# Kernel optimization log

Measured on AMD Instinct MI355X. Metric: run time of the kernel, lower is better.

The kernel has to match this reference:

```python
import jax, jax.numpy as jnp
import numpy as np

N_SKU, N_WH, N_SUP = 100000, 5000, 2000
D_IN, D_OUT, H = 128, 64, 4
DH = D_OUT // H  # 16
E_INTRA, E_CROSS = 400000, 200000
EPS_LN = 1e-5


def setup_inputs() -> dict:
    key = jax.random.key(0)
    ks = jax.random.split(key, 40)
    f32 = jnp.float32

    def edges(k, E, n_src, n_dst):
        k1, k2 = jax.random.split(k)
        return jnp.stack([
            jax.random.randint(k1, (E,), 0, n_src),
            jax.random.randint(k2, (E,), 0, n_dst),
        ]).astype(jnp.int32)

    inp = {
        'x_sku': jax.random.normal(ks[0], (N_SKU, D_IN), f32),
        'x_wh': jax.random.normal(ks[1], (N_WH, D_IN), f32),
        'x_sup': jax.random.normal(ks[2], (N_SUP, D_IN), f32),
    }
    names = ['plant', 'pg', 'sg', 'st', 'ship', 'supply']
    for i, nm in enumerate(names):
        inp['W_' + nm] = jax.random.normal(ks[3 + 2 * i], (D_IN, D_OUT), f32) * 0.05
        inp['a_' + nm] = jax.random.normal(ks[4 + 2 * i], (2 * DH,), f32) * 0.05
    inp['proj_W'] = jax.random.normal(ks[20], (2 * D_OUT, D_OUT), f32) * 0.05
    inp['proj_b'] = jnp.zeros((D_OUT,), f32)
    inp['ln_g'] = jnp.ones((D_OUT,), f32)
    inp['ln_b'] = jnp.zeros((D_OUT,), f32)
    inp['res_W'] = jax.random.normal(ks[21], (D_IN, D_OUT), f32) * 0.05
    inp['ei_plant'] = edges(ks[22], E_INTRA, N_SKU, N_SKU)
    inp['ei_pg'] = edges(ks[23], E_INTRA, N_SKU, N_SKU)
    inp['ei_sg'] = edges(ks[24], E_INTRA, N_SKU, N_SKU)
    inp['ei_st'] = edges(ks[25], E_INTRA, N_SKU, N_SKU)
    inp['ei_ship'] = edges(ks[26], E_CROSS, N_SKU, N_WH)
    inp['ei_supply'] = edges(ks[27], E_CROSS, N_SKU, N_SUP)
    return inp


def _gat_conv(src_feat, dst_feat, ei, W, a, num_dst):
    """One-edge-type multi-head GAT: ELU edge scores, per-dst softmax, scatter-add."""
    src_i, dst_i = ei[0], ei[1]
    h_src = (src_feat @ W).reshape(-1, H, DH)  # [N_src, H, dh]
    h_dst = (dst_feat @ W).reshape(-1, H, DH)  # [N_dst, H, dh]
    hs = h_src[src_i]  # [E, H, dh] gather
    hd = h_dst[dst_i]  # [E, H, dh]
    # a^T [h_src || h_dst], shared attention vector across heads
    e = jax.nn.elu(hs @ a[:DH] + hd @ a[DH:])  # [E, H]
    # numerically stable scatter-softmax over edges grouped by dst node
    e_max = jax.lax.stop_gradient(jax.ops.segment_max(e, dst_i, num_segments=num_dst))
    e_max = jnp.where(jnp.isfinite(e_max), e_max, 0.0)
    exp_e = jnp.exp(e - e_max[dst_i])
    denom = jax.ops.segment_sum(exp_e, dst_i, num_segments=num_dst)
    alpha = exp_e / (denom[dst_i] + 1e-12)  # [E, H]
    out = jax.ops.segment_sum(alpha[..., None] * hs, dst_i, num_segments=num_dst)
    return out.reshape(num_dst, D_OUT)


def reference(x_sku, x_wh, x_sup,
              W_plant, a_plant, W_pg, a_pg, W_sg, a_sg, W_st, a_st,
              W_ship, a_ship, W_supply, a_supply,
              proj_W, proj_b, ln_g, ln_b, res_W,
              ei_plant, ei_pg, ei_sg, ei_st, ei_ship, ei_supply):
    # branch A (intra sku->sku edge types), summed into sku accumulator
    oa_sku = (_gat_conv(x_sku, x_sku, ei_plant, W_plant, a_plant, N_SKU)
              + _gat_conv(x_sku, x_sku, ei_pg, W_pg, a_pg, N_SKU)
              + _gat_conv(x_sku, x_sku, ei_sg, W_sg, a_sg, N_SKU)
              + _gat_conv(x_sku, x_sku, ei_st, W_st, a_st, N_SKU))
    ob_sku = jnp.zeros((N_SKU, D_OUT), x_sku.dtype)
    # branch B (cross edge types)
    oa_wh = jnp.zeros((N_WH, D_OUT), x_wh.dtype)
    ob_wh = _gat_conv(x_sku, x_wh, ei_ship, W_ship, a_ship, N_WH)
    oa_sup = jnp.zeros((N_SUP, D_OUT), x_sup.dtype)
    ob_sup = _gat_conv(x_sku, x_sup, ei_supply, W_supply, a_supply, N_SUP)

    def finish(x, oa, ob):
        y = jnp.concatenate([oa, ob], axis=-1) @ proj_W + proj_b + x @ res_W
        mu = y.mean(-1, keepdims=True)
        var = ((y - mu) ** 2).mean(-1, keepdims=True)
        return (y - mu) / jnp.sqrt(var + EPS_LN) * ln_g + ln_b

    return (finish(x_sku, oa_sku, ob_sku),
            finish(x_wh, oa_wh, ob_wh),
            finish(x_sup, oa_sup, ob_sup))
```

## Files before the change

### kernel.cpp

```cpp
#include <hip/hip_runtime.h>
#include <hip/hip_bf16.h>
#include <cstdint>

#define NS 100000
#define NW 5000
#define NPS 2000
#define DI 128
#define DO 64
#define NSTRIPS (NS/16)
#define NFLAT (4*NS + NW + NPS)
#define NWPAD 5008
#define NBUK 134
#define BCAP 20480
#define CHUNK 8192

typedef unsigned short bfu;
typedef __attribute__((ext_vector_type(8))) short s8v;
typedef __attribute__((ext_vector_type(4))) float f4v;

__device__ inline bfu f2bf(float f) {
  uint32_t u = __float_as_uint(f);
  u = (u + 0x7FFFu + ((u >> 16) & 1u)) >> 16;
  return (bfu)u;
}
__device__ inline float bf2f(bfu u) {
  return __uint_as_float((uint32_t)u << 16);
}

__global__ void k_convert3(const float* __restrict__ x0, bfu* __restrict__ o0, int n0,
                           const float* __restrict__ x1, bfu* __restrict__ o1, int n1,
                           const float* __restrict__ x2, bfu* __restrict__ o2, int n2) {
  int t = blockIdx.x * 256 + threadIdx.x;
  const float* x; bfu* o; int i;
  if (t < n0) { x = x0; o = o0; i = t; }
  else if (t < n0 + n1) { x = x1; o = o1; i = t - n0; }
  else if (t < n0 + n1 + n2) { x = x2; o = o2; i = t - n0 - n1; }
  else return;
  const float4* p = (const float4*)x + (size_t)i * 2;
  float4 a = p[0], b = p[1];
  uint4 v;
  v.x = (uint32_t)f2bf(a.x) | ((uint32_t)f2bf(a.y) << 16);
  v.y = (uint32_t)f2bf(a.z) | ((uint32_t)f2bf(a.w) << 16);
  v.z = (uint32_t)f2bf(b.x) | ((uint32_t)f2bf(b.y) << 16);
  v.w = (uint32_t)f2bf(b.z) | ((uint32_t)f2bf(b.w) << 16);
  ((uint4*)o)[i] = v;
}

struct PackArgs {
  const float* W[6]; const float* a[6];
  const float* resW; const float* projW;
  bfu* Bp; bfu* Rp; bfu* Pp;
  float* wv_wh; float* wv_sup;
};
__global__ void k_pack_all(PackArgs P) {
  int t = blockIdx.x * 256 + threadIdx.x;
  if (t < 61440) {
    int ty = t / 10240, rem = t % 10240;
    int r = rem / 128, k = rem % 128;
    const float* W = P.W[ty]; const float* a = P.a[ty];
    float v = 0.f;
    if (r < 64) v = W[k * 64 + r];
    else if (r < 72) {
      int h = (r - 64) & 3;
      const float* av = (r < 68) ? a : (a + 16);
      #pragma unroll
      for (int m = 0; m < 16; ++m) v += W[k * 64 + h * 16 + m] * av[m];
    }
    P.Bp[ty * 10240 + rem] = f2bf(v);
  } else if (t < 69632) {
    int i = t - 61440; int j = i / 128, k = i % 128;
    P.Rp[i] = f2bf(P.resW[k * 64 + j]);
  } else if (t < 77824) {
    int i = t - 69632; int j = i / 128, k = i % 128;
    P.Pp[i] = f2bf(P.projW[k * 64 + j]);
  } else if (t < 78848) {
    int i = t - 77824; int which = i / 512;
    int k = (i % 512) / 4, h = i % 4;
    const float* W = P.W[4 + which]; const float* a = P.a[4 + which];
    float v = 0.f;
    #pragma unroll
    for (int m = 0; m < 16; ++m) v += W[k * 64 + h * 16 + m] * a[16 + m];
    (which ? P.wv_sup : P.wv_wh)[k * 4 + h] = v;
  }
}

__global__ __launch_bounds__(256, 2) void k_gemm2t(const bfu* __restrict__ xb,
    const bfu* __restrict__ Bp0, const bfu* __restrict__ Bp1,
    bfu* __restrict__ hb0, bfu* __restrict__ hb1,
    float* __restrict__ ss0, float* __restrict__ ss1,
    float* __restrict__ sd0, float* __restrict__ sd1, int nstrips) {
  int lane = threadIdx.x & 63;
  int l15 = lane & 15, q = lane >> 4;
  int w  = (int)((blockIdx.x * blockDim.x + threadIdx.x) >> 6);
  int nw = (int)((gridDim.x * blockDim.x) >> 6);
  s8v bfr[10][4];
  #pragma unroll
  for (int nt = 0; nt < 5; ++nt)
    #pragma unroll
    for (int kq = 0; kq < 4; ++kq) {
      bfr[nt][kq]     = *(const s8v*)(Bp0 + (size_t)(nt * 16 + l15) * 128 + kq * 32 + q * 8);
      bfr[5 + nt][kq] = *(const s8v*)(Bp1 + (size_t)(nt * 16 + l15) * 128 + kq * 32 + q * 8);
    }
  for (int s = w; s < nstrips; s += nw) {
    int mb = s * 16;
    f4v acc[10];
    #pragma unroll
    for (int u = 0; u < 10; ++u) acc[u] = (f4v){0.f, 0.f, 0.f, 0.f};
    const bfu* ar = xb + (size_t)(mb + l15) * 128 + q * 8;
    #pragma unroll
    for (int kq = 0; kq < 4; ++kq) {
      s8v af = *(const s8v*)(ar + kq * 32);
      #pragma unroll
      for (int u = 0; u < 10; ++u)
        acc[u] = __builtin_amdgcn_mfma_f32_16x16x32_bf16(af, bfr[u][kq], acc[u], 0, 0, 0);
    }
    #pragma unroll
    for (int u = 0; u < 10; ++u) {
      int nt = (u < 5) ? u : u - 5;
      bfu* hb = (u < 5) ? hb0 : hb1;
      float* ssrc = (u < 5) ? ss0 : ss1;
      float* sdst = (u < 5) ? sd0 : sd1;
      int c = nt * 16 + l15;
      #pragma unroll
      for (int r = 0; r < 4; ++r) {
        int node = mb + q * 4 + r;
        float v = acc[u][r];
        if (c < 64)      hb[(size_t)node * 64 + c] = f2bf(v);
        else if (c < 68) ssrc[(size_t)node * 4 + (c - 64)] = v;
        else if (c < 72) sdst[(size_t)node * 4 + (c - 68)] = v;
      }
    }
  }
}

__global__ __launch_bounds__(256) void k_scores(const float* __restrict__ x,
    const float* __restrict__ wv, float* __restrict__ sdst, int N) {
  int lane = threadIdx.x & 63;
  int w  = (int)((blockIdx.x * 256 + threadIdx.x) >> 6);
  int nw = (int)((gridDim.x * 256) >> 6);
  float4 wa = ((const float4*)wv)[lane];
  float4 wb = ((const float4*)wv)[64 + lane];
  for (int n = w; n < N; n += nw) {
    float xa = x[(size_t)n * 128 + lane], xc = x[(size_t)n * 128 + 64 + lane];
    float4 a;
    a.x = xa * wa.x + xc * wb.x; a.y = xa * wa.y + xc * wb.y;
    a.z = xa * wa.z + xc * wb.z; a.w = xa * wa.w + xc * wb.w;
    #pragma unroll
    for (int m = 1; m < 64; m <<= 1) {
      a.x += __shfl_xor(a.x, m); a.y += __shfl_xor(a.y, m);
      a.z += __shfl_xor(a.z, m); a.w += __shfl_xor(a.w, m);
    }
    if (lane == 0) ((float4*)sdst)[n] = a;
  }
}

struct ESeg { const int* ei[6]; int E[6]; int Ecum[7]; };

__device__ inline void buk_of(int t, int d, int& b, int& loc) {
  if (t < 4)       { int f = d * 4 + t; b = f >> 12;        loc = f & 4095; }
  else if (t == 4) { b = 98 + (d >> 8);                     loc = d & 255; }
  else             { b = 118 + (d >> 7);                    loc = d & 127; }
}

__global__ void k_init_cur(int* __restrict__ gCur) {
  int t = threadIdx.x;
  if (t < NBUK) gCur[t] = t * BCAP;
}

__global__ __launch_bounds__(256) void k_bin(ESeg S, int* __restrict__ gCur,
                                             uint32_t* __restrict__ binned, int ETOT) {
  __shared__ int cnt[NBUK];
  __shared__ int runb[NBUK];
  int tid = threadIdx.x;
  int gbase = blockIdx.x * CHUNK;
  if (tid < NBUK) cnt[tid] = 0;
  __syncthreads();
  #pragma unroll 4
  for (int i = 0; i < CHUNK / 256; ++i) {
    int g = gbase + i * 256 + tid;
    if (g < ETOT) {
      int t = 0;
      #pragma unroll
      for (int k = 0; k < 5; ++k) t += (g >= S.Ecum[k + 1]);
      int e = g - S.Ecum[t];
      int d = S.ei[t][S.E[t] + e];
      int b, loc; buk_of(t, d, b, loc);
      atomicAdd(&cnt[b], 1);
    }
  }
  __syncthreads();
  if (tid < NBUK) { runb[tid] = atomicAdd(&gCur[tid], cnt[tid]); cnt[tid] = 0; }
  __syncthreads();
  #pragma unroll 4
  for (int i = 0; i < CHUNK / 256; ++i) {
    int g = gbase + i * 256 + tid;
    if (g < ETOT) {
      int t = 0;
      #pragma unroll
      for (int k = 0; k < 5; ++k) t += (g >= S.Ecum[k + 1]);
      int e = g - S.Ecum[t];
      int sv = S.ei[t][e];
      int d  = S.ei[t][S.E[t] + e];
      int b, loc; buk_of(t, d, b, loc);
      int pos = runb[b] + atomicAdd(&cnt[b], 1);
      if (pos < (b + 1) * BCAP)
        binned[pos] = ((uint32_t)loc << 17) | (uint32_t)sv;
    }
  }
}

__global__ __launch_bounds__(1024) void k_csr(const int* __restrict__ gCur,
    const uint32_t* __restrict__ binned, int* __restrict__ offs,
    int* __restrict__ ssorted) {
  __shared__ int hist[4096];
  __shared__ int wsc[16];
  __shared__ int bbase_s, cnt_s;
  int b = blockIdx.x, tid = threadIdx.x;
  int lane = tid & 63, wid = tid >> 6;
  if (tid == 0) {
    int bb = 0, own = 0;
    for (int k = 0; k < NBUK; ++k) {
      int c = min(gCur[k] - k * BCAP, BCAP);
      if (k < b) bb += c;
      if (k == b) own = c;
    }
    bbase_s = bb; cnt_s = own;
  }
  #pragma unroll
  for (int k = 0; k < 4; ++k) hist[tid * 4 + k] = 0;
  __syncthreads();
  int cnt = cnt_s, bbase = bbase_s;
  const uint32_t* bk = binned + (size_t)b * BCAP;
  for (int i = tid; i < cnt; i += 1024)
    atomicAdd(&hist[bk[i] >> 17], 1);
  __syncthreads();
  int t4 = tid * 4;
  int v0 = hist[t4], v1 = hist[t4 + 1], v2 = hist[t4 + 2], v3 = hist[t4 + 3];
  int tsum = v0 + v1 + v2 + v3;
  int inc = tsum;
  #pragma unroll
  for (int d = 1; d < 64; d <<= 1) { int tt = __shfl_up(inc, d); if (lane >= d) inc += tt; }
  if (lane == 63) wsc[wid] = inc;
  __syncthreads();
  int wpre = 0;
  for (int k = 0; k < wid; ++k) wpre += wsc[k];
  int excl = inc - tsum + wpre;
  hist[t4] = excl;
  hist[t4 + 1] = excl + v0;
  hist[t4 + 2] = excl + v0 + v1;
  hist[t4 + 3] = excl + v0 + v1 + v2;
  __syncthreads();
  int sbase, nslots;
  if (b < 98)        { sbase = b << 12;                nslots = min(4096, 4 * NS - sbase); }
  else if (b < 118)  { int lb = (b - 98) << 8;  sbase = 4 * NS + lb;      nslots = min(256, NW - lb); }
  else               { int lb = (b - 118) << 7; sbase = 4 * NS + NW + lb; nslots = min(128, NPS - lb); }
  for (int i = tid; i < nslots; i += 1024) offs[sbase + i] = bbase + hist[i];
  if (b == NBUK - 1 && tid == 0) offs[NFLAT] = bbase + cnt;
  __syncthreads();
  for (int i = tid; i < cnt; i += 1024) {
    uint32_t v = bk[i];
    int p = atomicAdd(&hist[v >> 17], 1);
    ssorted[bbase + p] = (int)(v & 0x1FFFFu);
  }
}

struct AggArgs {
  const int* offs; const int* srcs;
  const bfu* hbAll;
  const float* ssAll;
  const float* sdAll;
  const float* sd_wh; const float* sd_sup;
  bfu* osku; bfu* owh; bfu* osup;
};

__global__ __launch_bounds__(256) void k_megaagg(AggArgs A) {
  int lane = threadIdx.x & 63, h = lane >> 4;
  int w  = (int)((blockIdx.x * 256 + threadIdx.x) >> 6);
  int nw = (int)((gridDim.x * 256) >> 6);
  for (int n = w; n < NS + NW + NPS; n += nw) {
    float r; bfu* op;
    if (n < NS) {
      const int* ob = A.offs + (size_t)n * 4;
      int4 o = *(const int4*)ob;
      int o4 = ob[4];
      int beg = o.x;
      int b1 = o.y - beg, b2 = o.z - beg, b3 = o.w - beg;
      int tot = o4 - beg;
      float sdv0 = A.sdAll[(size_t)(0 * NS + n) * 4 + h];
      float sdv1 = A.sdAll[(size_t)(1 * NS + n) * 4 + h];
      float sdv2 = A.sdAll[(size_t)(2 * NS + n) * 4 + h];
      float sdv3 = A.sdAll[(size_t)(3 * NS + n) * 4 + h];
      float acc0 = 0.f, acc1 = 0.f, acc2 = 0.f, acc3 = 0.f;
      float den0 = 0.f, den1 = 0.f, den2 = 0.f, den3 = 0.f;
      for (int cb = 0; cb < tot; cb += 64) {
        int rem = min(64, tot - cb);
        int sidx = (lane < rem) ? A.srcs[beg + cb + lane] : 0;
        int j = 0;
        for (; j + 8 <= rem; j += 8) {
          float sc[8]; bfu hv[8]; int tv[8];
          #pragma unroll
          for (int i = 0; i < 8; ++i) {
            int p = cb + j + i;
            int t = (p >= b1) + (p >= b2) + (p >= b3);
            int s = __shfl(sidx, j + i);
            size_t nb = (size_t)t * NS + s;
            sc[i] = A.ssAll[nb * 4 + h];
            hv[i] = A.hbAll[nb * 64 + lane];
            tv[i] = t;
          }
          #pragma unroll
          for (int i = 0; i < 8; ++i) {
            float sdv = (tv[i] == 0) ? sdv0 : (tv[i] == 1) ? sdv1 : (tv[i] == 2) ? sdv2 : sdv3;
            float e = sc[i] + sdv;
            e = e > 0.f ? e : (__expf(e) - 1.f);
            float wgt = __expf(e);
            float hw = bf2f(hv[i]) * wgt;
            if (tv[i] == 0)      { den0 += wgt; acc0 += hw; }
            else if (tv[i] == 1) { den1 += wgt; acc1 += hw; }
            else if (tv[i] == 2) { den2 += wgt; acc2 += hw; }
            else                 { den3 += wgt; acc3 += hw; }
          }
        }
        for (; j < rem; ++j) {
          int p = cb + j;
          int t = (p >= b1) + (p >= b2) + (p >= b3);
          int s = __shfl(sidx, j);
          size_t nb = (size_t)t * NS + s;
          float sc = A.ssAll[nb * 4 + h];
          float hvf = bf2f(A.hbAll[nb * 64 + lane]);
          float sdv = (t == 0) ? sdv0 : (t == 1) ? sdv1 : (t == 2) ? sdv2 : sdv3;
          float e = sc + sdv;
          e = e > 0.f ? e : (__expf(e) - 1.f);
          float wgt = __expf(e);
          float hw = hvf * wgt;
          if (t == 0)      { den0 += wgt; acc0 += hw; }
          else if (t == 1) { den1 += wgt; acc1 += hw; }
          else if (t == 2) { den2 += wgt; acc2 += hw; }
          else             { den3 += wgt; acc3 += hw; }
        }
      }
      r = acc0 / (den0 + 1e-12f) + acc1 / (den1 + 1e-12f)
        + acc2 / (den2 + 1e-12f) + acc3 / (den3 + 1e-12f);
      op = A.osku + (size_t)n * 64;
    } else {
      int tt, nl, fi; const float* sd;
      if (n < NS + NW) { tt = 4; nl = n - NS; fi = 4 * NS + nl; sd = A.sd_wh; op = A.owh + (size_t)nl * 64; }
      else { tt = 5; nl = n - NS - NW; fi = 4 * NS + NW + nl; sd = A.sd_sup; op = A.osup + (size_t)nl * 64; }
      int beg = A.offs[fi], end = A.offs[fi + 1];
      const bfu* hb = A.hbAll + (size_t)tt * NS * 64;
      const float* ss = A.ssAll + (size_t)tt * NS * 4;
      float sdv = sd[(size_t)nl * 4 + h];
      float acc = 0.f, den = 0.f;
      for (int cb = beg; cb < end; cb += 64) {
        int rem = min(64, end - cb);
        int sidx = (lane < rem) ? A.srcs[cb + lane] : 0;
        int j = 0;
        for (; j + 8 <= rem; j += 8) {
          float sc[8]; bfu hv[8];
          #pragma unroll
          for (int i = 0; i < 8; ++i) {
            int s = __shfl(sidx, j + i);
            sc[i] = ss[(size_t)s * 4 + h];
            hv[i] = hb[(size_t)s * 64 + lane];
          }
          #pragma unroll
          for (int i = 0; i < 8; ++i) {
            float e = sc[i] + sdv;
            e = e > 0.f ? e : (__expf(e) - 1.f);
            float wgt = __expf(e);
            den += wgt; acc += bf2f(hv[i]) * wgt;
          }
        }
        for (; j < rem; ++j) {
          int s = __shfl(sidx, j);
          float e = ss[(size_t)s * 4 + h] + sdv;
          float hvf = bf2f(hb[(size_t)s * 64 + lane]);
          e = e > 0.f ? e : (__expf(e) - 1.f);
          float wgt = __expf(e);
          den += wgt; acc += hvf * wgt;
        }
      }
      r = acc / (den + 1e-12f);
    }
    op[lane] = f2bf(r);
  }
}

__global__ __launch_bounds__(256) void k_finishM(const bfu* __restrict__ aggb,
    const bfu* __restrict__ xbf, const bfu* __restrict__ Pp, int koff,
    const bfu* __restrict__ Rp, const float* __restrict__ pb,
    const float* __restrict__ g, const float* __restrict__ bb,
    float* __restrict__ outp, int N, int nstrips) {
  int lane = threadIdx.x & 63, l15 = lane & 15, q = lane >> 4;
  int w  = (int)((blockIdx.x * 256 + threadIdx.x) >> 6);
  int nw = (int)((gridDim.x * 256) >> 6);
  s8v bP[4][2], bR[4][4];
  float pbv[4], gv[4], bv[4];
  #pragma unroll
  for (int c = 0; c < 4; ++c) {
    const bfu* pr = Pp + (size_t)(c * 16 + l15) * 128 + koff;
    bP[c][0] = *(const s8v*)(pr + q * 8);
    bP[c][1] = *(const s8v*)(pr + 32 + q * 8);
    const bfu* rr = Rp + (size_t)(c * 16 + l15) * 128;
    #pragma unroll
    for (int kq = 0; kq < 4; ++kq) bR[c][kq] = *(const s8v*)(rr + kq * 32 + q * 8);
    pbv[c] = pb[c * 16 + l15]; gv[c] = g[c * 16 + l15]; bv[c] = bb[c * 16 + l15];
  }
  for (int s = w; s < nstrips; s += nw) {
    int mb = s * 16;
    const bfu* ar = aggb + (size_t)(mb + l15) * 64 + q * 8;
    const bfu* xr = xbf + (size_t)(mb + l15) * 128 + q * 8;
    s8v a0 = *(const s8v*)ar, a1 = *(const s8v*)(ar + 32);
    s8v x0 = *(const s8v*)xr, x1 = *(const s8v*)(xr + 32),
        x2 = *(const s8v*)(xr + 64), x3 = *(const s8v*)(xr + 96);
    f4v acc[4];
    #pragma unroll
    for (int c = 0; c < 4; ++c) {
      acc[c] = (f4v){0.f, 0.f, 0.f, 0.f};
      acc[c] = __builtin_amdgcn_mfma_f32_16x16x32_bf16(a0, bP[c][0], acc[c], 0, 0, 0);
      acc[c] = __builtin_amdgcn_mfma_f32_16x16x32_bf16(a1, bP[c][1], acc[c], 0, 0, 0);
      acc[c] = __builtin_amdgcn_mfma_f32_16x16x32_bf16(x0, bR[c][0], acc[c], 0, 0, 0);
      acc[c] = __builtin_amdgcn_mfma_f32_16x16x32_bf16(x1, bR[c][1], acc[c], 0, 0, 0);
      acc[c] = __builtin_amdgcn_mfma_f32_16x16x32_bf16(x2, bR[c][2], acc[c], 0, 0, 0);
      acc[c] = __builtin_amdgcn_mfma_f32_16x16x32_bf16(x3, bR[c][3], acc[c], 0, 0, 0);
    }
    #pragma unroll
    for (int r = 0; r < 4; ++r) {
      int row = mb + q * 4 + r;
      float y0 = acc[0][r] + pbv[0], y1 = acc[1][r] + pbv[1];
      float y2 = acc[2][r] + pbv[2], y3 = acc[3][r] + pbv[3];
      float s1 = y0 + y1 + y2 + y3;
      s1 += __shfl_xor(s1, 1); s1 += __shfl_xor(s1, 2);
      s1 += __shfl_xor(s1, 4); s1 += __shfl_xor(s1, 8);
      float mu = s1 * 0.015625f;
      float d0 = y0 - mu, d1 = y1 - mu, d2 = y2 - mu, d3 = y3 - mu;
      float s2 = d0 * d0 + d1 * d1 + d2 * d2 + d3 * d3;
      s2 += __shfl_xor(s2, 1); s2 += __shfl_xor(s2, 2);
      s2 += __shfl_xor(s2, 4); s2 += __shfl_xor(s2, 8);
      float rs = rsqrtf(s2 * 0.015625f + 1e-5f);
      if (row < N) {
        float* orow = outp + (size_t)row * 64 + l15;
        orow[0]  = d0 * rs * gv[0] + bv[0];
        orow[16] = d1 * rs * gv[1] + bv[1];
        orow[32] = d2 * rs * gv[2] + bv[2];
        orow[48] = d3 * rs * gv[3] + bv[3];
      }
    }
  }
}

extern "C" void kernel_launch(void* const* d_in, const int* in_sizes, int n_in,
                              void* d_out, int out_size, void* d_ws, size_t ws_size,
                              hipStream_t stream) {
  const float* x_sku = (const float*)d_in[0];
  const float* x_wh  = (const float*)d_in[1];
  const float* x_sup = (const float*)d_in[2];
  const float* Wt[6]; const float* at[6];
  for (int t = 0; t < 6; ++t) { Wt[t] = (const float*)d_in[3 + 2 * t]; at[t] = (const float*)d_in[4 + 2 * t]; }
  const float* projW = (const float*)d_in[15];
  const float* projb = (const float*)d_in[16];
  const float* lng   = (const float*)d_in[17];
  const float* lnb   = (const float*)d_in[18];
  const float* resW  = (const float*)d_in[19];
  const int* ei[6]; int Et[6];
  for (int t = 0; t < 6; ++t) { ei[t] = (const int*)d_in[20 + t]; Et[t] = in_sizes[20 + t] / 2; }
  float* out = (float*)d_out;

  int ETOT = 0;
  for (int t = 0; t < 6; ++t) ETOT += Et[t];

  char* ws = (char*)d_ws;
  size_t off = 0;
  auto alloc = [&](size_t bytes) { off = (off + 255) & ~(size_t)255; void* p = ws + off; off += bytes; return p; };

  bfu*  xb      = (bfu*)alloc((size_t)NS * DI * 2);
  bfu*  xb_wh   = (bfu*)alloc((size_t)NWPAD * DI * 2);
  bfu*  xb_sup  = (bfu*)alloc((size_t)NPS * DI * 2);
  bfu*  Bp      = (bfu*)alloc((size_t)6 * 80 * 128 * 2);
  bfu*  Rp      = (bfu*)alloc((size_t)64 * 128 * 2);
  bfu*  Pp      = (bfu*)alloc((size_t)64 * 128 * 2);
  float* wv_wh  = (float*)alloc(128 * 4 * 4);
  float* wv_sup = (float*)alloc(128 * 4 * 4);
  bfu*  hbAll   = (bfu*)alloc((size_t)6 * NS * 64 * 2);
  float* ssAll  = (float*)alloc((size_t)6 * NS * 4 * 4);
  float* sdAll  = (float*)alloc((size_t)6 * NS * 4 * 4);
  float* sdst_wh  = (float*)alloc((size_t)NW * 4 * 4);
  float* sdst_sup = (float*)alloc((size_t)NPS * 4 * 4);
  size_t agg_bytes = ((size_t)NS + NWPAD + NPS) * 64 * 2;
  size_t bin_bytes = (size_t)NBUK * BCAP * 4;
  char* un = (char*)alloc(agg_bytes > bin_bytes ? agg_bytes : bin_bytes);
  bfu* agg_sku = (bfu*)un;
  bfu* agg_wh  = agg_sku + (size_t)NS * 64;
  bfu* agg_sup = agg_wh + (size_t)NWPAD * 64;
  uint32_t* binned = (uint32_t*)un;
  int* gCur    = (int*)alloc(256 * 4);
  int* offsb   = (int*)alloc((size_t)(NFLAT + 1) * 4);
  int* ssorted = (int*)alloc((size_t)ETOT * 4);

  int n0 = NS * 16, n1 = NW * 16, n2 = NPS * 16;
  k_convert3<<<(n0 + n1 + n2 + 255) / 256, 256, 0, stream>>>(x_sku, xb, n0, x_wh, xb_wh, n1,
                                                             x_sup, xb_sup, n2);

  PackArgs PA;
  for (int t = 0; t < 6; ++t) { PA.W[t] = Wt[t]; PA.a[t] = at[t]; }
  PA.resW = resW; PA.projW = projW; PA.Bp = Bp; PA.Rp = Rp; PA.Pp = Pp;
  PA.wv_wh = wv_wh; PA.wv_sup = wv_sup;
  k_pack_all<<<(78848 + 255) / 256, 256, 0, stream>>>(PA);

  k_scores<<<1250, 256, 0, stream>>>(x_wh, wv_wh, sdst_wh, NW);
  k_scores<<<500, 256, 0, stream>>>(x_sup, wv_sup, sdst_sup, NPS);

  ESeg S;
  S.Ecum[0] = 0;
  for (int t = 0; t < 6; ++t) { S.ei[t] = ei[t]; S.E[t] = Et[t]; S.Ecum[t + 1] = S.Ecum[t] + Et[t]; }
  k_init_cur<<<1, 256, 0, stream>>>(gCur);
  k_bin<<<(ETOT + CHUNK - 1) / CHUNK, 256, 0, stream>>>(S, gCur, binned, ETOT);
  k_csr<<<NBUK, 1024, 0, stream>>>(gCur, binned, offsb, ssorted);

  for (int p = 0; p < 3; ++p) {
    int t0 = 2 * p, t1 = 2 * p + 1;
    k_gemm2t<<<512, 256, 0, stream>>>(xb, Bp + (size_t)t0 * 10240, Bp + (size_t)t1 * 10240,
        hbAll + (size_t)t0 * NS * 64, hbAll + (size_t)t1 * NS * 64,
        ssAll + (size_t)t0 * NS * 4, ssAll + (size_t)t1 * NS * 4,
        sdAll + (size_t)t0 * NS * 4, sdAll + (size_t)t1 * NS * 4, NSTRIPS);
  }

  AggArgs A;
  A.offs = offsb; A.srcs = ssorted;
  A.hbAll = hbAll; A.ssAll = ssAll; A.sdAll = sdAll;
  A.sd_wh = sdst_wh; A.sd_sup = sdst_sup;
  A.osku = agg_sku; A.owh = agg_wh; A.osup = agg_sup;
  k_megaagg<<<(NS + NW + NPS + 3) / 4, 256, 0, stream>>>(A);

  k_finishM<<<1563, 256, 0, stream>>>(agg_sku, xb, Pp, 0, Rp, projb, lng, lnb, out, NS, NSTRIPS);
  k_finishM<<<79, 256, 0, stream>>>(agg_wh, xb_wh, Pp, 64, Rp, projb, lng, lnb,
                                    out + (size_t)NS * 64, NW, NWPAD / 16);
  k_finishM<<<32, 256, 0, stream>>>(agg_sup, xb_sup, Pp, 64, Rp, projb, lng, lnb,
                                    out + (size_t)(NS + NW) * 64, NPS, NPS / 16);
}
```

Before: 464.6 us.

## Split wavefront into quarter-waves processing edge types in parallel with vector loads

The aggregation kernel now maps each 16-lane quarter of a wavefront to one edge type (for SKU nodes) or to interleaved edges (for cross nodes). Each lane loads four bf16 features at once via uint2 and accumulates four channels, and partial sums are combined with cross-quarter shuffles. This replaces the per-edge type selection and serial walk over all edges with four concurrent streams of wider gathers. The cost is padding up to the longest edge-type list, predicated work on short lists, and an extra shuffle reduction at the end.

```diff
diff --git a/kernel.cpp b/kernel.cpp
--- a/kernel.cpp
+++ b/kernel.cpp
@@ -274,115 +274,112 @@
 };
 
 __global__ __launch_bounds__(256) void k_megaagg(AggArgs A) {
-  int lane = threadIdx.x & 63, h = lane >> 4;
+  int lane = threadIdx.x & 63;
+  int q = lane >> 4, m = lane & 15, h = m >> 2;
+  int qsh = q << 4;
   int w  = (int)((blockIdx.x * 256 + threadIdx.x) >> 6);
   int nw = (int)((gridDim.x * 256) >> 6);
   for (int n = w; n < NS + NW + NPS; n += nw) {
-    float r; bfu* op;
     if (n < NS) {
       const int* ob = A.offs + (size_t)n * 4;
       int4 o = *(const int4*)ob;
       int o4 = ob[4];
-      int beg = o.x;
-      int b1 = o.y - beg, b2 = o.z - beg, b3 = o.w - beg;
-      int tot = o4 - beg;
-      float sdv0 = A.sdAll[(size_t)(0 * NS + n) * 4 + h];
-      float sdv1 = A.sdAll[(size_t)(1 * NS + n) * 4 + h];
-      float sdv2 = A.sdAll[(size_t)(2 * NS + n) * 4 + h];
-      float sdv3 = A.sdAll[(size_t)(3 * NS + n) * 4 + h];
-      float acc0 = 0.f, acc1 = 0.f, acc2 = 0.f, acc3 = 0.f;
-      float den0 = 0.f, den1 = 0.f, den2 = 0.f, den3 = 0.f;
-      for (int cb = 0; cb < tot; cb += 64) {
-        int rem = min(64, tot - cb);
-        int sidx = (lane < rem) ? A.srcs[beg + cb + lane] : 0;
-        int j = 0;
-        for (; j + 8 <= rem; j += 8) {
-          float sc[8]; bfu hv[8]; int tv[8];
+      int sb = (q == 0) ? o.x : (q == 1) ? o.y : (q == 2) ? o.z : o.w;
+      int se = (q == 0) ? o.y : (q == 1) ? o.z : (q == 2) ? o.w : o4;
+      int len = se - sb;
+      int maxlen = max(max(o.y - o.x, o.z - o.y), max(o.w - o.z, o4 - o.w));
+      float sdv = A.sdAll[((size_t)q * NS + n) * 4 + h];
+      uint32_t tbase = (uint32_t)q * (uint32_t)NS;
+      float den = 0.f, a0 = 0.f, a1 = 0.f, a2 = 0.f, a3 = 0.f;
+      for (int j0 = 0; j0 < maxlen; j0 += 16) {
+        int ei = j0 + m;
+        int sidx = (ei < len) ? A.srcs[sb + ei] : 0;
+        int gmax = min(16, maxlen - j0);
+        for (int jj = 0; jj < gmax; jj += 8) {
+          float sc[8]; uint2 hv[8]; int vj[8];
           #pragma unroll
           for (int i = 0; i < 8; ++i) {
-            int p = cb + j + i;
-            int t = (p >= b1) + (p >= b2) + (p >= b3);
-            int s = __shfl(sidx, j + i);
-            size_t nb = (size_t)t * NS + s;
-            sc[i] = A.ssAll[nb * 4 + h];
-            hv[i] = A.hbAll[nb * 64 + lane];
-            tv[i] = t;
-          }
-          #pragma unroll
-          for (int i = 0; i < 8; ++i) {
-            float sdv = (tv[i] == 0) ? sdv0 : (tv[i] == 1) ? sdv1 : (tv[i] == 2) ? sdv2 : sdv3;
-            float e = sc[i] + sdv;
-            e = e > 0.f ? e : (__expf(e) - 1.f);
-            float wgt = __expf(e);
-            float hw = bf2f(hv[i]) * wgt;
-            if (tv[i] == 0)      { den0 += wgt; acc0 += hw; }
-            else if (tv[i] == 1) { den1 += wgt; acc1 += hw; }
-            else if (tv[i] == 2) { den2 += wgt; acc2 += hw; }
-            else                 { den3 += wgt; acc3 += hw; }
-          }
-        }
-        for (; j < rem; ++j) {
-          int p = cb + j;
-          int t = (p >= b1) + (p >= b2) + (p >= b3);
-          int s = __shfl(sidx, j);
-          size_t nb = (size_t)t * NS + s;
-          float sc = A.ssAll[nb * 4 + h];
-          float hvf = bf2f(A.hbAll[nb * 64 + lane]);
-          float sdv = (t == 0) ? sdv0 : (t == 1) ? sdv1 : (t == 2) ? sdv2 : sdv3;
-          float e = sc + sdv;
-          e = e > 0.f ? e : (__expf(e) - 1.f);
-          float wgt = __expf(e);
-          float hw = hvf * wgt;
-          if (t == 0)      { den0 += wgt; acc0 += hw; }
-          else if (t == 1) { den1 += wgt; acc1 += hw; }
-          else if (t == 2) { den2 += wgt; acc2 += hw; }
-          else             { den3 += wgt; acc3 += hw; }
-        }
-      }
-      r = acc0 / (den0 + 1e-12f) + acc1 / (den1 + 1e-12f)
-        + acc2 / (den2 + 1e-12f) + acc3 / (den3 + 1e-12f);
-      op = A.osku + (size_t)n * 64;
-    } else {
-      int tt, nl, fi; const float* sd;
-      if (n < NS + NW) { tt = 4; nl = n - NS; fi = 4 * NS + nl; sd = A.sd_wh; op = A.owh + (size_t)nl * 64; }
-      else { tt = 5; nl = n - NS - NW; fi = 4 * NS + NW + nl; sd = A.sd_sup; op = A.osup + (size_t)nl * 64; }
-      int beg = A.offs[fi], end = A.offs[fi + 1];
-      const bfu* hb = A.hbAll + (size_t)tt * NS * 64;
-      const float* ss = A.ssAll + (size_t)tt * NS * 4;
-      float sdv = sd[(size_t)nl * 4 + h];
-      float acc = 0.f, den = 0.f;
-      for (int cb = beg; cb < end; cb += 64) {
-        int rem = min(64, end - cb);
-        int sidx = (lane < rem) ? A.srcs[cb + lane] : 0;
-        int j = 0;
-        for (; j + 8 <= rem; j += 8) {
-          float sc[8]; bfu hv[8];
-          #pragma unroll
-          for (int i = 0; i < 8; ++i) {
-            int s = __shfl(sidx, j + i);
-            sc[i] = ss[(size_t)s * 4 + h];
-            hv[i] = hb[(size_t)s * 64 + lane];
+            int j = jj + i;
+            int s = __shfl(sidx, qsh + j);
+            vj[i] = (j0 + j) < len;
+            uint32_t nb = tbase + (uint32_t)s;
+            sc[i] = A.ssAll[nb * 4u + (uint32_t)h];
+            hv[i] = *(const uint2*)(A.hbAll + nb * 64u + (uint32_t)(m * 4));
           }
           #pragma unroll
           for (int i = 0; i < 8; ++i) {
             float e = sc[i] + sdv;
             e = e > 0.f ? e : (__expf(e) - 1.f);
-            float wgt = __expf(e);
-            den += wgt; acc += bf2f(hv[i]) * wgt;
+            float wgt = vj[i] ? __expf(e) : 0.f;
+            den += wgt;
+            a0 = fmaf(__uint_as_float(hv[i].x << 16), wgt, a0);
+            a1 = fmaf(__uint_as_float(hv[i].x & 0xffff0000u), wgt, a1);
+            a2 = fmaf(__uint_as_float(hv[i].y << 16), wgt, a2);
+            a3 = fmaf(__uint_as_float(hv[i].y & 0xffff0000u), wgt, a3);
           }
         }
-        for (; j < rem; ++j) {
-          int s = __shfl(sidx, j);
-          float e = ss[(size_t)s * 4 + h] + sdv;
-          float hvf = bf2f(hb[(size_t)s * 64 + lane]);
-          e = e > 0.f ? e : (__expf(e) - 1.f);
-          float wgt = __expf(e);
-          den += wgt; acc += hvf * wgt;
+      }
+      float inv = __builtin_amdgcn_rcpf(den + 1e-12f);
+      float r0 = a0 * inv, r1 = a1 * inv, r2 = a2 * inv, r3 = a3 * inv;
+      r0 += __shfl_xor(r0, 16); r0 += __shfl_xor(r0, 32);
+      r1 += __shfl_xor(r1, 16); r1 += __shfl_xor(r1, 32);
+      r2 += __shfl_xor(r2, 16); r2 += __shfl_xor(r2, 32);
+      r3 += __shfl_xor(r3, 16); r3 += __shfl_xor(r3, 32);
+      if (q == 0) {
+        uint2 pk;
+        pk.x = (uint32_t)f2bf(r0) | ((uint32_t)f2bf(r1) << 16);
+        pk.y = (uint32_t)f2bf(r2) | ((uint32_t)f2bf(r3) << 16);
+        *(uint2*)(A.osku + (size_t)n * 64 + m * 4) = pk;
+      }
+    } else {
+      int tt, nl; const float* sd; bfu* op;
+      int fi;
+      if (n < NS + NW) { tt = 4; nl = n - NS; fi = 4 * NS + nl; sd = A.sd_wh; op = A.owh + (size_t)nl * 64; }
+      else { tt = 5; nl = n - NS - NW; fi = 4 * NS + NW + nl; sd = A.sd_sup; op = A.osup + (size_t)nl * 64; }
+      int beg = A.offs[fi], end = A.offs[fi + 1];
+      uint32_t tbase = (uint32_t)tt * (uint32_t)NS;
+      float sdv = sd[(size_t)nl * 4 + h];
+      float den = 0.f, a0 = 0.f, a1 = 0.f, a2 = 0.f, a3 = 0.f;
+      for (int cb = beg; cb < end; cb += 64) {
+        int rem = min(64, end - cb);
+        int sidx = (lane < rem) ? A.srcs[cb + lane] : 0;
+        for (int jb = 0; jb < rem; jb += 32) {
+          float sc[8]; uint2 hv[8]; int vj[8];
+          #pragma unroll
+          for (int i = 0; i < 8; ++i) {
+            int eidx = jb + 4 * i + q;
+            int s = __shfl(sidx, eidx);
+            vj[i] = eidx < rem;
+            uint32_t nb = tbase + (uint32_t)s;
+            sc[i] = A.ssAll[nb * 4u + (uint32_t)h];
+            hv[i] = *(const uint2*)(A.hbAll + nb * 64u + (uint32_t)(m * 4));
+          }
+          #pragma unroll
+          for (int i = 0; i < 8; ++i) {
+            float e = sc[i] + sdv;
+            e = e > 0.f ? e : (__expf(e) - 1.f);
+            float wgt = vj[i] ? __expf(e) : 0.f;
+            den += wgt;
+            a0 = fmaf(__uint_as_float(hv[i].x << 16), wgt, a0);
+            a1 = fmaf(__uint_as_float(hv[i].x & 0xffff0000u), wgt, a1);
+            a2 = fmaf(__uint_as_float(hv[i].y << 16), wgt, a2);
+            a3 = fmaf(__uint_as_float(hv[i].y & 0xffff0000u), wgt, a3);
+          }
         }
       }
-      r = acc / (den + 1e-12f);
-    }
-    op[lane] = f2bf(r);
+      den += __shfl_xor(den, 16); den += __shfl_xor(den, 32);
+      a0 += __shfl_xor(a0, 16); a0 += __shfl_xor(a0, 32);
+      a1 += __shfl_xor(a1, 16); a1 += __shfl_xor(a1, 32);
+      a2 += __shfl_xor(a2, 16); a2 += __shfl_xor(a2, 32);
+      a3 += __shfl_xor(a3, 16); a3 += __shfl_xor(a3, 32);
+      float inv = __builtin_amdgcn_rcpf(den + 1e-12f);
+      if (q == 0) {
+        uint2 pk;
+        pk.x = (uint32_t)f2bf(a0 * inv) | ((uint32_t)f2bf(a1 * inv) << 16);
+        pk.y = (uint32_t)f2bf(a2 * inv) | ((uint32_t)f2bf(a3 * inv) << 16);
+        *(uint2*)(op + m * 4) = pk;
+      }
+    }
   }
 }
 
```

Measured after the change: 416.1 us. 10.4% less time.
